# Kernel tuning notes

Measured on AMD Instinct MI355X. Metric: run time of the kernel, lower is better.

The kernel has to match this reference:

```python
import jax, jax.numpy as jnp
import numpy as np

B, S, H, E = 4, 4096, 4096, 64
TOP_K = 2


def setup_inputs() -> dict:
    key = jax.random.key(0)
    k1, k2 = jax.random.split(key)
    x = jax.random.normal(k1, (B, S, H), dtype=jnp.float32)
    # nn.Linear weight: [num_experts, hidden_size]
    gate_w = jax.random.normal(k2, (E, H), dtype=jnp.float32) * (1.0 / np.sqrt(H))
    return {"x": x, "gate_w": gate_w}


def reference(x, gate_w):
    # gate linear: [B,S,H] @ [H,E] -> [B,S,E]
    router_logits = jnp.einsum("bsh,eh->bse", x, gate_w)
    router_weights = jax.nn.softmax(router_logits, axis=-1)
    topk_weights, topk_indices = jax.lax.top_k(router_weights, TOP_K)  # [B,S,2]
    topk_weights = topk_weights / jnp.sum(topk_weights, axis=-1, keepdims=True)
    return topk_weights, topk_indices
```

## Files before the change

### kernel.cpp

```cpp
#include <hip/hip_runtime.h>
#include <math.h>


typedef _Float16 half8 __attribute__((ext_vector_type(8)));
typedef float floatx4 __attribute__((ext_vector_type(4)));

constexpr int Hdim = 4096;
constexpr int Edim = 64;
constexpr int NTOK = 16384;
constexpr int BK   = 128;
constexpr int NKT  = Hdim / BK;
constexpr float SCL  = 2048.0f;
constexpr float ISCL = 1.0f / 2048.0f;

#define GLD_LDS16(gp, lp)                                              \
    __builtin_amdgcn_global_load_lds(                                  \
        (const __attribute__((address_space(1))) void*)(gp),           \
        (__attribute__((address_space(3))) void*)(lp), 16, 0, 0)

__global__ __launch_bounds__(256)
void wconv_kernel(const float* __restrict__ gw,
                  _Float16* __restrict__ whf,
                  _Float16* __restrict__ wlf)
{
    const int n    = blockIdx.x * 256 + threadIdx.x;
    const int lane = n & 63;
    const int frag = n >> 6;
    const int nt   = frag & 3;
    const int kc   = frag >> 2;
    const int e    = nt * 16 + (lane & 15);
    const int k0   = kc * 32 + (lane >> 4) * 8;

    const float* src = gw + (size_t)e * Hdim + k0;
    const float4 v0 = *(const float4*)src;
    const float4 v1 = *(const float4*)(src + 4);
    const float* p0 = (const float*)&v0;
    const float* p1 = (const float*)&v1;
    half8 h, l;
    #pragma unroll
    for (int c = 0; c < 4; ++c) {
        _Float16 hh = (_Float16)p0[c];
        h[c] = hh;
        l[c] = (_Float16)((p0[c] - (float)hh) * SCL);
        hh = (_Float16)p1[c];
        h[c + 4] = hh;
        l[c + 4] = (_Float16)((p1[c] - (float)hh) * SCL);
    }
    *(half8*)(whf + (size_t)n * 8) = h;
    *(half8*)(wlf + (size_t)n * 8) = l;
}

__global__ __launch_bounds__(256, 4)
void router_kernel(const float* __restrict__ x,
                   const _Float16* __restrict__ whf,
                   const _Float16* __restrict__ wlf,
                   float* __restrict__ out)
{
    __shared__ alignas(16) float  sx[2][16 * BK];
    __shared__ alignas(16) float4 sc[4][16];

    const int tid  = threadIdx.x;
    const int w    = tid >> 6;
    const int lane = tid & 63;
    const int ln15 = lane & 15;
    const int quad = lane >> 4;
    const int sw   = ln15 & 7;
    const int t0   = blockIdx.x * 16;

    const int r0 = w * 4 + (lane >> 5);
    const int r1 = r0 + 2;
    const int g0 = (lane & 31) ^ (r0 & 7);
    const int g1 = (lane & 31) ^ (r1 & 7);
    const float* px0 = x + (size_t)(t0 + r0) * Hdim + g0 * 4;
    const float* px1 = x + (size_t)(t0 + r1) * Hdim + g1 * 4;

    const _Float16* whw = whf + (size_t)w * 512 + lane * 8;
    const _Float16* wlw = wlf + (size_t)w * 512 + lane * 8;

    floatx4 accm = (floatx4)0.0f, accc = (floatx4)0.0f, accl = (floatx4)0.0f;

    auto cvt8 = [&](const float4& a, const float4& b, half8& h, half8& l) {
        const float* pa = (const float*)&a;
        const float* pb = (const float*)&b;
        #pragma unroll
        for (int c = 0; c < 4; ++c) {
            _Float16 hh = (_Float16)pa[c];
            h[c] = hh;
            l[c] = (_Float16)((pa[c] - (float)hh) * SCL);
            hh = (_Float16)pb[c];
            h[c + 4] = hh;
            l[c + 4] = (_Float16)((pb[c] - (float)hh) * SCL);
        }
    };

    GLD_LDS16(px0, &sx[0][w * 512]);
    GLD_LDS16(px1, &sx[0][w * 512 + 256]);
    px0 += BK; px1 += BK;
    __syncthreads();

    for (int kt = 0; kt < NKT; ++kt) {
        const int cur = kt & 1;
        if (kt + 1 < NKT) {
            GLD_LDS16(px0, &sx[cur ^ 1][w * 512]);
            GLD_LDS16(px1, &sx[cur ^ 1][w * 512 + 256]);
            px0 += BK; px1 += BK;
        }

        half8 bh[4], bl[4];
        #pragma unroll
        for (int c = 0; c < 4; ++c) {
            const size_t kc = (size_t)(kt * 4 + c) * 2048;
            bh[c] = *(const half8*)(whw + kc);
            bl[c] = *(const half8*)(wlw + kc);
        }

        #pragma unroll
        for (int c = 0; c < 4; ++c) {
            const int s0 = (c * 8 + quad * 2) ^ sw;
            const float4 f0 = *(const float4*)&sx[cur][ln15 * BK + s0 * 4];
            const float4 f1 = *(const float4*)&sx[cur][ln15 * BK + (s0 ^ 1) * 4];
            half8 ah, al;
            cvt8(f0, f1, ah, al);
            accm = __builtin_amdgcn_mfma_f32_16x16x32_f16(ah, bh[c], accm, 0, 0, 0);
            accc = __builtin_amdgcn_mfma_f32_16x16x32_f16(ah, bl[c], accc, 0, 0, 0);
            accc = __builtin_amdgcn_mfma_f32_16x16x32_f16(al, bh[c], accc, 0, 0, 0);
            accl = __builtin_amdgcn_mfma_f32_16x16x32_f16(al, bl[c], accl, 0, 0, 0);
        }
        __syncthreads();
    }

    const floatx4 vv = accm + accc * ISCL + accl * (ISCL * ISCL);

    #pragma unroll
    for (int i = 0; i < 4; ++i) {
        float m1 = vv[i], m2 = -INFINITY;
        int i1 = w * 16 + ln15, i2 = 0;
        #pragma unroll
        for (int mk = 1; mk <= 8; mk <<= 1) {
            const float om1 = __shfl_xor(m1, mk);
            const int   oi1 = __shfl_xor(i1, mk);
            const float om2 = __shfl_xor(m2, mk);
            const int   oi2 = __shfl_xor(i2, mk);
            const bool aw = (m1 > om1) || (m1 == om1 && i1 < oi1);
            const float w1v = aw ? m1 : om1;  const int w1i = aw ? i1 : oi1;
            const float ca  = aw ? m2 : om2;  const int cai = aw ? i2 : oi2;
            const float cb  = aw ? om1 : m1;  const int cbi = aw ? oi1 : i1;
            const bool sw2 = (ca > cb) || (ca == cb && cai < cbi);
            m1 = w1v; i1 = w1i;
            m2 = sw2 ? ca : cb;
            i2 = sw2 ? cai : cbi;
        }
        if (ln15 == 0)
            sc[w][quad * 4 + i] = float4{m1, m2, (float)i1, (float)i2};
    }
    __syncthreads();

    if (tid < 16) {
        float4 c = sc[0][tid];
        float m1 = c.x, m2 = c.y, i1 = c.z, i2 = c.w;
        #pragma unroll
        for (int q = 1; q < 4; ++q) {
            c = sc[q][tid];
            const float om1 = c.x, om2 = c.y, oi1 = c.z, oi2 = c.w;
            const bool aw = (m1 > om1) || (m1 == om1 && i1 < oi1);
            const float w1v = aw ? m1 : om1;  const float w1i = aw ? i1 : oi1;
            const float ca  = aw ? m2 : om2;  const float cai = aw ? i2 : oi2;
            const float cb  = aw ? om1 : m1;  const float cbi = aw ? oi1 : i1;
            const bool sw2 = (ca > cb) || (ca == cb && cai < cbi);
            m1 = w1v; i1 = w1i;
            m2 = sw2 ? ca : cb;
            i2 = sw2 ? cai : cbi;
        }
        const float r   = expf(m2 - m1);
        const float inv = 1.0f / (1.0f + r);
        const int t = t0 + tid;
        float* ow = out + 2 * (size_t)t;
        ow[0] = inv;
        ow[1] = r * inv;
        float* oi = out + 2 * (size_t)NTOK + 2 * (size_t)t;
        oi[0] = i1;
        oi[1] = i2;
    }
}

extern "C" void kernel_launch(void* const* d_in, const int* in_sizes, int n_in,
                              void* d_out, int out_size, void* d_ws, size_t ws_size,
                              hipStream_t stream) {
    const float* x  = (const float*)d_in[0];
    const float* gw = (const float*)d_in[1];
    float* out = (float*)d_out;
    _Float16* whf = (_Float16*)d_ws;
    _Float16* wlf = whf + (size_t)Edim * Hdim;

    hipLaunchKernelGGL(wconv_kernel, dim3(128), dim3(256), 0, stream, gw, whf, wlf);
    hipLaunchKernelGGL(router_kernel, dim3(NTOK / 16), dim3(256), 0, stream,
                       x, whf, wlf, out);
}
```

Before: 382.2 us.

## Convert x tile to split fp16 once per block in LDS, shared by all waves

Before, each of the four waves converted the same 16xBK fp32 x tile into hi/lo fp16 halves on its own, so the conversion was done four times. Now all 256 threads split the conversion, each converting 8 values, and write the hi/lo halves to new swizzled LDS buffers that the waves then read directly as MFMA operands. This removes redundant VALU conversion work. In exchange it adds an extra __syncthreads per k-step and uses more LDS, which may reduce occupancy or add sync stalls.

```diff
diff --git a/kernel.cpp b/kernel.cpp
--- a/kernel.cpp
+++ b/kernel.cpp
@@ -56,15 +56,16 @@
                    const _Float16* __restrict__ wlf,
                    float* __restrict__ out)
 {
-    __shared__ alignas(16) float  sx[2][16 * BK];
-    __shared__ alignas(16) float4 sc[4][16];
+    __shared__ alignas(16) float    sx[2][16 * BK];
+    __shared__ alignas(16) _Float16 sxh[2][16 * BK];
+    __shared__ alignas(16) _Float16 sxl[2][16 * BK];
+    __shared__ alignas(16) float4   sc[4][16];
 
     const int tid  = threadIdx.x;
     const int w    = tid >> 6;
     const int lane = tid & 63;
     const int ln15 = lane & 15;
     const int quad = lane >> 4;
-    const int sw   = ln15 & 7;
     const int t0   = blockIdx.x * 16;
 
     const int r0 = w * 4 + (lane >> 5);
@@ -74,24 +75,17 @@
     const float* px0 = x + (size_t)(t0 + r0) * Hdim + g0 * 4;
     const float* px1 = x + (size_t)(t0 + r1) * Hdim + g1 * 4;
 
+    const int trow = tid & 15;
+    const int tg   = tid >> 4;
+    const int tsw  = trow & 7;
+    const int rdA  = trow * BK + (((2 * tg)     ^ tsw) << 2);
+    const int rdB  = trow * BK + (((2 * tg + 1) ^ tsw) << 2);
+    const int wrS  = trow * BK + ((tg ^ tsw) << 3);
+
     const _Float16* whw = whf + (size_t)w * 512 + lane * 8;
     const _Float16* wlw = wlf + (size_t)w * 512 + lane * 8;
 
     floatx4 accm = (floatx4)0.0f, accc = (floatx4)0.0f, accl = (floatx4)0.0f;
-
-    auto cvt8 = [&](const float4& a, const float4& b, half8& h, half8& l) {
-        const float* pa = (const float*)&a;
-        const float* pb = (const float*)&b;
-        #pragma unroll
-        for (int c = 0; c < 4; ++c) {
-            _Float16 hh = (_Float16)pa[c];
-            h[c] = hh;
-            l[c] = (_Float16)((pa[c] - (float)hh) * SCL);
-            hh = (_Float16)pb[c];
-            h[c + 4] = hh;
-            l[c + 4] = (_Float16)((pb[c] - (float)hh) * SCL);
-        }
-    };
 
     GLD_LDS16(px0, &sx[0][w * 512]);
     GLD_LDS16(px1, &sx[0][w * 512 + 256]);
@@ -100,6 +94,27 @@
 
     for (int kt = 0; kt < NKT; ++kt) {
         const int cur = kt & 1;
+
+        {
+            const float4 f0 = *(const float4*)&sx[cur][rdA];
+            const float4 f1 = *(const float4*)&sx[cur][rdB];
+            const float* pa = (const float*)&f0;
+            const float* pb = (const float*)&f1;
+            half8 h, l;
+            #pragma unroll
+            for (int c = 0; c < 4; ++c) {
+                _Float16 hh = (_Float16)pa[c];
+                h[c] = hh;
+                l[c] = (_Float16)((pa[c] - (float)hh) * SCL);
+                hh = (_Float16)pb[c];
+                h[c + 4] = hh;
+                l[c + 4] = (_Float16)((pb[c] - (float)hh) * SCL);
+            }
+            *(half8*)&sxh[cur][wrS] = h;
+            *(half8*)&sxl[cur][wrS] = l;
+        }
+        __syncthreads();
+
         if (kt + 1 < NKT) {
             GLD_LDS16(px0, &sx[cur ^ 1][w * 512]);
             GLD_LDS16(px1, &sx[cur ^ 1][w * 512 + 256]);
@@ -116,11 +131,9 @@
 
         #pragma unroll
         for (int c = 0; c < 4; ++c) {
-            const int s0 = (c * 8 + quad * 2) ^ sw;
-            const float4 f0 = *(const float4*)&sx[cur][ln15 * BK + s0 * 4];
-            const float4 f1 = *(const float4*)&sx[cur][ln15 * BK + (s0 ^ 1) * 4];
-            half8 ah, al;
-            cvt8(f0, f1, ah, al);
+            const int sA = ln15 * BK + (((4 * c + quad) ^ (ln15 & 7)) << 3);
+            const half8 ah = *(const half8*)&sxh[cur][sA];
+            const half8 al = *(const half8*)&sxl[cur][sA];
             accm = __builtin_amdgcn_mfma_f32_16x16x32_f16(ah, bh[c], accm, 0, 0, 0);
             accc = __builtin_amdgcn_mfma_f32_16x16x32_f16(ah, bl[c], accc, 0, 0, 0);
             accc = __builtin_amdgcn_mfma_f32_16x16x32_f16(al, bh[c], accc, 0, 0, 0);
```

Measured after the change: 396.5 us. 3.7% more time.

## Triple-buffer x tiles and register double-buffer weight fragments with manual waitcnt

Applied to the files above, without the earlier changes.

Moves the x staging from a double buffer to a triple buffer in LDS, so global-to-LDS loads run two k-tiles ahead. Weight fragments are prefetched one k-tile ahead into alternating register sets. __syncthreads is replaced with explicit s_waitcnt vmcnt and s_barrier, and a sched_barrier pins the instruction order. The aim is to hide global memory latency behind the MFMA work, at the cost of more registers and LDS, tighter hand-managed counters, and redundant wraparound loads in the last iterations.

```diff
diff --git a/kernel.cpp b/kernel.cpp
--- a/kernel.cpp
+++ b/kernel.cpp
@@ -56,7 +56,7 @@
                    const _Float16* __restrict__ wlf,
                    float* __restrict__ out)
 {
-    __shared__ alignas(16) float  sx[2][16 * BK];
+    __shared__ alignas(16) float  sx[3][16 * BK];
     __shared__ alignas(16) float4 sc[4][16];
 
     const int tid  = threadIdx.x;
@@ -93,27 +93,37 @@
         }
     };
 
-    GLD_LDS16(px0, &sx[0][w * 512]);
-    GLD_LDS16(px1, &sx[0][w * 512 + 256]);
-    px0 += BK; px1 += BK;
-    __syncthreads();
-
-    for (int kt = 0; kt < NKT; ++kt) {
-        const int cur = kt & 1;
-        if (kt + 1 < NKT) {
-            GLD_LDS16(px0, &sx[cur ^ 1][w * 512]);
-            GLD_LDS16(px1, &sx[cur ^ 1][w * 512 + 256]);
-            px0 += BK; px1 += BK;
-        }
-
-        half8 bh[4], bl[4];
+    half8 bhA[4], blA[4], bhB[4], blB[4];
+
+    #pragma unroll
+    for (int c = 0; c < 4; ++c) {
+        bhA[c] = *(const half8*)(whw + (size_t)c * 2048);
+        blA[c] = *(const half8*)(wlw + (size_t)c * 2048);
+    }
+    GLD_LDS16(px0,      &sx[0][w * 512]);
+    GLD_LDS16(px1,      &sx[0][w * 512 + 256]);
+    GLD_LDS16(px0 + BK, &sx[1][w * 512]);
+    GLD_LDS16(px1 + BK, &sx[1][w * 512 + 256]);
+
+    auto step = [&](int kt, half8 (&bch)[4], half8 (&bcl)[4],
+                            half8 (&bnh)[4], half8 (&bnl)[4]) {
+        const int ktn = (kt + 1) & (NKT - 1);
         #pragma unroll
         for (int c = 0; c < 4; ++c) {
-            const size_t kc = (size_t)(kt * 4 + c) * 2048;
-            bh[c] = *(const half8*)(whw + kc);
-            bl[c] = *(const half8*)(wlw + kc);
-        }
-
+            bnh[c] = *(const half8*)(whw + (size_t)(ktn * 4 + c) * 2048);
+            bnl[c] = *(const half8*)(wlw + (size_t)(ktn * 4 + c) * 2048);
+        }
+        __builtin_amdgcn_sched_barrier(0);
+
+        const int ts = (kt + 2) & (NKT - 1);
+        const int tb = (kt + 2) % 3;
+        GLD_LDS16(px0 + (size_t)ts * BK, &sx[tb][w * 512]);
+        GLD_LDS16(px1 + (size_t)ts * BK, &sx[tb][w * 512 + 256]);
+
+        asm volatile("s_waitcnt vmcnt(12)" ::: "memory");
+        asm volatile("s_barrier" ::: "memory");
+
+        const int cur = kt % 3;
         #pragma unroll
         for (int c = 0; c < 4; ++c) {
             const int s0 = (c * 8 + quad * 2) ^ sw;
@@ -121,13 +131,19 @@
             const float4 f1 = *(const float4*)&sx[cur][ln15 * BK + (s0 ^ 1) * 4];
             half8 ah, al;
             cvt8(f0, f1, ah, al);
-            accm = __builtin_amdgcn_mfma_f32_16x16x32_f16(ah, bh[c], accm, 0, 0, 0);
-            accc = __builtin_amdgcn_mfma_f32_16x16x32_f16(ah, bl[c], accc, 0, 0, 0);
-            accc = __builtin_amdgcn_mfma_f32_16x16x32_f16(al, bh[c], accc, 0, 0, 0);
-            accl = __builtin_amdgcn_mfma_f32_16x16x32_f16(al, bl[c], accl, 0, 0, 0);
-        }
-        __syncthreads();
-    }
+            accm = __builtin_amdgcn_mfma_f32_16x16x32_f16(ah, bch[c], accm, 0, 0, 0);
+            accc = __builtin_amdgcn_mfma_f32_16x16x32_f16(ah, bcl[c], accc, 0, 0, 0);
+            accc = __builtin_amdgcn_mfma_f32_16x16x32_f16(al, bch[c], accc, 0, 0, 0);
+            accl = __builtin_amdgcn_mfma_f32_16x16x32_f16(al, bcl[c], accl, 0, 0, 0);
+        }
+        asm volatile("s_barrier" ::: "memory");
+    };
+
+    for (int kt = 0; kt < NKT; kt += 2) {
+        step(kt,     bhA, blA, bhB, blB);
+        step(kt + 1, bhB, blB, bhA, blA);
+    }
+    __syncthreads();
 
     const floatx4 vv = accm + accc * ISCL + accl * (ISCL * ISCL);
 
```

New measurement: 376.4 us. No clear change (-1.5%).
